# Kernel optimization log

Hardware: AMD Instinct MI355X
Metric: run time of the kernel (lower is better)

The kernel has to match this reference:

```python
import jax, jax.numpy as jnp
import numpy as np

B, S, D, H = 32, 128, 64, 4
HD = D // H            # head dim 16
HT = 4 * D             # hidden_t_dim = 256
TE = 4 * HT            # time_embed_dim = 1024
V = 1024               # vocab
STEP = 0.1             # step_size (Lie-Trotter step)


def setup_inputs():
    key = jax.random.key(0)
    ks = jax.random.split(key, 12)
    n = lambda k, shp: 0.02 * jax.random.normal(k, shp, jnp.float32)
    return dict(
        inputs_idx=jax.random.randint(ks[0], (B, S), 0, V),
        num_loops=100,
        wte=n(ks[1], (V, D)),
        wpe=n(ks[2], (S, D)),
        t_w1=n(ks[3], (HT, TE)), t_b1=jnp.zeros((TE,), jnp.float32),
        t_w2=n(ks[4], (TE, D)), t_b2=jnp.zeros((D,), jnp.float32),
        ln1_g=jnp.ones((D,), jnp.float32), ln1_b=jnp.zeros((D,), jnp.float32),
        w_qkv=n(ks[5], (D, 3 * D)), b_qkv=jnp.zeros((3 * D,), jnp.float32),
        w_o=n(ks[6], (D, D)), b_o=jnp.zeros((D,), jnp.float32),
        ln2_g=jnp.ones((D,), jnp.float32), ln2_b=jnp.zeros((D,), jnp.float32),
        w_fc=n(ks[7], (D, 4 * D)), b_fc=jnp.zeros((4 * D,), jnp.float32),
        w_pr=n(ks[8], (4 * D, D)), b_pr=jnp.zeros((D,), jnp.float32),
        lnf_g=jnp.ones((D,), jnp.float32), lnf_b=jnp.zeros((D,), jnp.float32),
    )


def _ln(x, g, b, eps=1e-5):
    mu = jnp.mean(x, axis=-1, keepdims=True)
    var = jnp.var(x, axis=-1, keepdims=True)
    return (x - mu) * jax.lax.rsqrt(var + eps) * g + b


def _timestep_embedding(t, dim):
    # sinusoidal (diffusion-style) embedding of scalar step index t -> (dim,)
    half = dim // 2
    freqs = jnp.exp(-np.log(10000.0) * jnp.arange(half, dtype=jnp.float32) / half)
    args = t * freqs
    return jnp.concatenate([jnp.cos(args), jnp.sin(args)], axis=-1)


def reference(inputs_idx, num_loops, wte, wpe, t_w1, t_b1, t_w2, t_b2,
              ln1_g, ln1_b, w_qkv, b_qkv, w_o, b_o,
              ln2_g, ln2_b, w_fc, b_fc, w_pr, b_pr, lnf_g, lnf_b):
    x = wte[inputs_idx] + wpe[jnp.arange(S)]          # (B,S,D)
    neg_inf = jnp.float32(-1e9)
    cmask = jnp.where(jnp.tril(jnp.ones((S, S), bool)), 0.0, neg_inf)  # causal
    scale = 1.0 / np.sqrt(HD)

    def step(x, t):
        # shared time embedding added to state each loop iteration
        te = _timestep_embedding(t, HT)
        temb = jax.nn.silu(te @ t_w1 + t_b1) @ t_w2 + t_b2   # (D,)
        x = x + temb
        # pre-norm attention, Lie-Trotter sub-step
        h = _ln(x, ln1_g, ln1_b)
        qkv = h @ w_qkv + b_qkv                               # (B,S,3D)
        q, k, v = jnp.split(qkv, 3, axis=-1)
        q = q.reshape(B, S, H, HD)
        k = k.reshape(B, S, H, HD)
        v = v.reshape(B, S, H, HD)
        att = jnp.einsum('bqhd,bkhd->bhqk', q, k) * scale + cmask
        att = jax.nn.softmax(att, axis=-1)
        a = jnp.einsum('bhqk,bkhd->bqhd', att, v).reshape(B, S, D)
        x = x + STEP * (a @ w_o + b_o)
        # pre-norm MLP, second sub-step
        h = _ln(x, ln2_g, ln2_b)
        m = jax.nn.gelu(h @ w_fc + b_fc) @ w_pr + b_pr
        x = x + STEP * m
        return x, None

    ts = jnp.arange(num_loops, dtype=jnp.float32)
    x, _ = jax.lax.scan(step, x, ts)
    return _ln(x, lnf_g, lnf_b)
```

## Files before the change

kernel.cpp:

```cpp
#include <hip/hip_runtime.h>
#include <hip/hip_bf16.h>
#include <math.h>

#define BB   32
#define SS   128
#define DD   64
#define HTT  256
#define TEE  1024
#define NTHR 512
#define XST  68
#define STEPF 0.1f

typedef __attribute__((ext_vector_type(8))) short short8b;
typedef __attribute__((ext_vector_type(4))) float float4v;

__device__ __forceinline__ unsigned short f2b(float f) {
    union { float f; unsigned int u; } x; x.f = f;
    unsigned int u = x.u + 0x7FFFu + ((x.u >> 16) & 1u);
    return (unsigned short)(u >> 16);
}

__global__ void pack_frags(const float* __restrict__ w_qkv,
                           const float* __restrict__ w_o,
                           const float* __restrict__ w_fc,
                           const float* __restrict__ w_pr,
                           unsigned short* __restrict__ frags) {
    const int tile = blockIdx.x;
    const int t = threadIdx.x;
    const int lane = t >> 3, e = t & 7;
    const float* W; int N, nt, ks;
    if (tile < 24)      { W = w_qkv; N = 192; int s = tile;      nt = s >> 1; ks = s & 1; }
    else if (tile < 32) { W = w_o;   N = 64;  int s = tile - 24; nt = s >> 1; ks = s & 1; }
    else if (tile < 64) { W = w_fc;  N = 256; int s = tile - 32; nt = s >> 1; ks = s & 1; }
    else                { W = w_pr;  N = 64;  int s = tile - 64; nt = s >> 3; ks = s & 7; }
    const int k   = ks * 32 + (lane >> 4) * 8 + e;
    const int col = nt * 16 + (lane & 15);
    frags[tile * 512 + lane * 8 + e] = f2b(W[k * N + col]);
}

__global__ void temb_precompute(const int* __restrict__ nloops_p,
                                const float* __restrict__ t_w1,
                                const float* __restrict__ t_b1,
                                const float* __restrict__ t_w2,
                                const float* __restrict__ t_b2,
                                float* __restrict__ tembBuf) {
    const int t = blockIdx.x;
    const int nl = nloops_p[0];
    if (t >= nl) return;

    __shared__ float te_s[HTT];
    __shared__ float h1[TEE];
    const int tid = threadIdx.x;
    const float tf = (float)t;

    {
        int fi = (tid < 128) ? tid : (tid - 128);
        float freq = expf(-9.210340371976184f * (float)fi * (1.0f / 128.0f));
        float arg = tf * freq;
        te_s[tid] = (tid < 128) ? cosf(arg) : sinf(arg);
    }
    __syncthreads();

    for (int j = tid; j < TEE; j += 256) {
        float acc = t_b1[j];
        for (int i = 0; i < HTT; ++i)
            acc = fmaf(te_s[i], t_w1[i * TEE + j], acc);
        h1[j] = acc / (1.0f + expf(-acc));
    }
    __syncthreads();

    {
        const int d = tid >> 2, part = tid & 3;
        float acc = 0.0f;
        for (int j = part; j < TEE; j += 4)
            acc = fmaf(h1[j], t_w2[j * DD + d], acc);
        acc += __shfl_xor(acc, 1);
        acc += __shfl_xor(acc, 2);
        if (part == 0) tembBuf[t * DD + d] = acc + t_b2[d];
    }
}

__device__ __forceinline__ float gelu_tanh(float u) {
    float z = 0.7978845608028654f * (u + 0.044715f * u * u * u);
    float e = __expf(2.0f * z);
    float th = 1.0f - 2.0f / (e + 1.0f);
    return 0.5f * u * (1.0f + th);
}

__global__ __launch_bounds__(NTHR, 2)
void looped_tf(const int* __restrict__ idx,
               const int* __restrict__ nloops_p,
               const float* __restrict__ wte,
               const float* __restrict__ wpe,
               const float* __restrict__ ln1_g, const float* __restrict__ ln1_b,
               const float* __restrict__ b_qkv,
               const float* __restrict__ b_o,
               const float* __restrict__ ln2_g, const float* __restrict__ ln2_b,
               const float* __restrict__ b_fc,
               const float* __restrict__ b_pr,
               const float* __restrict__ lnf_g, const float* __restrict__ lnf_b,
               const float* __restrict__ tembBuf,
               const unsigned short* __restrict__ frags,
               float* __restrict__ out) {
    __shared__ __align__(16) float xs[SS * XST];
    __shared__ __align__(16) unsigned short hsb[SS * DD];
    __shared__ __align__(16) unsigned char pool[66560];
    __shared__ __align__(16) unsigned short pstage[8 * 640];
    __shared__ __align__(16) unsigned short wfrag[16384];

    unsigned char* qb  = pool;
    unsigned char* kb  = pool + 24576;
    unsigned char* vtb = pool + 49152;
    unsigned short* msb = (unsigned short*)pool;

    const unsigned short* fcF = frags + 32 * 512;
    const unsigned short* prF = frags + 64 * 512;

    const int b   = blockIdx.x;
    const int tid = threadIdx.x;
    const int nl  = nloops_p[0];
    const int wv  = tid >> 6;
    const int ln  = tid & 63;
    const int fr  = ln & 15;
    const int fq  = ln >> 4;

    for (int i = tid; i < 2048; i += NTHR)
        ((int4*)wfrag)[i] = ((const int4*)frags)[i];

    for (int i = tid; i < SS * DD; i += NTHR) {
        int s = i >> 6, d = i & 63;
        xs[s * XST + d] = wte[idx[b * SS + s] * DD + d] + wpe[i];
    }
    __syncthreads();

    const int tok4 = tid >> 2, sub4 = tid & 3;

    auto ln_to_hsb = [&](const float* __restrict__ g, const float* __restrict__ be) {
        float v[16];
        const float* xp = xs + tok4 * XST + sub4 * 16;
        float s1 = 0.f, s2 = 0.f;
#pragma unroll
        for (int r = 0; r < 4; ++r) {
            float4 f = *(const float4*)(xp + 4 * r);
            v[4*r+0]=f.x; v[4*r+1]=f.y; v[4*r+2]=f.z; v[4*r+3]=f.w;
            s1 += f.x + f.y + f.z + f.w;
            s2 += f.x*f.x + f.y*f.y + f.z*f.z + f.w*f.w;
        }
        s1 += __shfl_xor(s1, 1); s2 += __shfl_xor(s2, 1);
        s1 += __shfl_xor(s1, 2); s2 += __shfl_xor(s2, 2);
        float mu = s1 * (1.0f / 64.0f);
        float var = s2 * (1.0f / 64.0f) - mu * mu;
        float rs = rsqrtf(var + 1e-5f);
        short8b p0, p1;
#pragma unroll
        for (int i = 0; i < 8; ++i) {
            int d2 = sub4 * 16 + i;
            p0[i] = (short)f2b((v[i] - mu) * rs * g[d2] + be[d2]);
        }
#pragma unroll
        for (int i = 0; i < 8; ++i) {
            int d2 = sub4 * 16 + 8 + i;
            p1[i] = (short)f2b((v[8+i] - mu) * rs * g[d2] + be[d2]);
        }
        const int row = tok4, swz = (row & 7) << 4;
        char* base = (char*)hsb;
        int b0 = row * 128 + sub4 * 32;
        *(short8b*)(base + (b0 ^ swz)) = p0;
        *(short8b*)(base + ((b0 + 16) ^ swz)) = p1;
    };

    auto load_afrag = [&](const unsigned short* buf, int rstrideB, int kstep) -> short8b {
        int row = wv * 16 + fr;
        int byte = row * rstrideB + kstep * 64 + fq * 16;
        return *(const short8b*)((const char*)buf + (byte ^ ((row & 7) << 4)));
    };

    for (int t = 0; t < nl; ++t) {
        for (int i = tid; i < SS * DD; i += NTHR)
            xs[(i >> 6) * XST + (i & 63)] += tembBuf[t * DD + (i & 63)];
        __syncthreads();

        ln_to_hsb(ln1_g, ln1_b);
        __syncthreads();

        {
            short8b a0 = load_afrag(hsb, 128, 0);
            short8b a1 = load_afrag(hsb, 128, 1);
            float4v acc[12];
#pragma unroll
            for (int nt = 0; nt < 12; ++nt) acc[nt] = (float4v)0.0f;
#pragma unroll
            for (int nt = 0; nt < 12; ++nt) {
                short8b b0 = *(const short8b*)(&wfrag[(nt * 2 + 0) * 512 + ln * 8]);
                short8b b1 = *(const short8b*)(&wfrag[(nt * 2 + 1) * 512 + ln * 8]);
                acc[nt] = __builtin_amdgcn_mfma_f32_16x16x32_bf16(a0, b0, acc[nt], 0, 0, 0);
                acc[nt] = __builtin_amdgcn_mfma_f32_16x16x32_bf16(a1, b1, acc[nt], 0, 0, 0);
            }
#pragma unroll
            for (int nt = 0; nt < 12; ++nt) {
                const int col = nt * 16 + fr;
                const float bias = b_qkv[col];
#pragma unroll
                for (int r = 0; r < 4; ++r) {
                    int row = wv * 16 + fq * 4 + r;
                    unsigned short bv = f2b(acc[nt][r] + bias);
                    if (nt < 4) {
                        int h = nt, d = fr;
                        int byte = h * 6144 + row * 48 + d * 2;
                        byte ^= ((row >> 3) & 7) << 4;
                        *(unsigned short*)(qb + byte) = bv;
                    } else if (nt < 8) {
                        int h = nt - 4, d = fr;
                        *(unsigned short*)(kb + h * 6144 + row * 48 + d * 2) = bv;
                    } else {
                        int h = nt - 8, d = fr;
                        *(unsigned short*)(vtb + h * 4352 + d * 272 + row * 2) = bv;
                    }
                }
            }
        }
        __syncthreads();

        {
            short8b aq[4];
            {
                bool lo = (ln < 32);
#pragma unroll
                for (int h = 0; h < 4; ++h) {
                    short8b z = (short8b)(short)0;
                    if (lo) {
                        int q = wv + 8 * fr;
                        int byte = h * 6144 + q * 48 + (fq & 1) * 16;
                        byte ^= (fr & 7) << 4;
                        z = *(const short8b*)(qb + byte);
                    }
                    aq[h] = z;
                }
            }
            short8b onesb;
#pragma unroll
            for (int e = 0; e < 8; ++e) onesb[e] = (short)0x3F80;

            float4v o[4], lac[4];
#pragma unroll
            for (int h = 0; h < 4; ++h) { o[h] = (float4v)0.0f; lac[h] = (float4v)0.0f; }

            unsigned short* pst = pstage + wv * 640;

            for (int ktp = 0; ktp < 4; ++ktp) {
#pragma unroll
                for (int h = 0; h < 4; ++h) {
                    short8b bk0 = (short8b)(short)0, bk1 = (short8b)(short)0;
                    if (ln < 32) {
                        int kbase = h * 6144 + (fq & 1) * 16;
                        bk0 = *(const short8b*)(kb + kbase + (ktp * 32 + fr) * 48);
                        bk1 = *(const short8b*)(kb + kbase + (ktp * 32 + 16 + fr) * 48);
                    }
                    float4v s0 = __builtin_amdgcn_mfma_f32_16x16x32_bf16(aq[h], bk0, (float4v)0.0f, 0, 0, 0);
                    float4v s1 = __builtin_amdgcn_mfma_f32_16x16x32_bf16(aq[h], bk1, (float4v)0.0f, 0, 0, 0);
#pragma unroll
                    for (int r = 0; r < 4; ++r) {
                        int j = 4 * fq + r;
                        int q = wv + 8 * j;
                        int kk0 = ktp * 32 + fr;
                        int kk1 = kk0 + 16;
                        float p0 = (kk0 <= q) ? __expf(s0[r] * 0.25f) : 0.0f;
                        float p1 = (kk1 <= q) ? __expf(s1[r] * 0.25f) : 0.0f;
                        pst[j * 40 + fr]      = f2b(p0);
                        pst[j * 40 + 16 + fr] = f2b(p1);
                    }
                    short8b ap = *(const short8b*)((const char*)pst + fr * 80 + fq * 16);
                    short8b bv = *(const short8b*)(vtb + h * 4352 + fr * 272 + ktp * 64 + fq * 16);
                    o[h]   = __builtin_amdgcn_mfma_f32_16x16x32_bf16(ap, bv, o[h], 0, 0, 0);
                    lac[h] = __builtin_amdgcn_mfma_f32_16x16x32_bf16(ap, onesb, lac[h], 0, 0, 0);
                }
            }
#pragma unroll
            for (int h = 0; h < 4; ++h) {
#pragma unroll
                for (int r = 0; r < 4; ++r) {
                    int j = 4 * fq + r;
                    int q = wv + 8 * j;
                    float val = o[h][r] / lac[h][r];
                    int byte = (q * 128 + (h * 16 + fr) * 2) ^ ((q & 7) << 4);
                    *(unsigned short*)((char*)hsb + byte) = f2b(val);
                }
            }
        }
        __syncthreads();

        {
            short8b a0 = load_afrag(hsb, 128, 0);
            short8b a1 = load_afrag(hsb, 128, 1);
            float4v acc[4];
#pragma unroll
            for (int nt = 0; nt < 4; ++nt) acc[nt] = (float4v)0.0f;
#pragma unroll
            for (int nt = 0; nt < 4; ++nt) {
                short8b b0 = *(const short8b*)(&wfrag[(24 + nt * 2 + 0) * 512 + ln * 8]);
                short8b b1 = *(const short8b*)(&wfrag[(24 + nt * 2 + 1) * 512 + ln * 8]);
                acc[nt] = __builtin_amdgcn_mfma_f32_16x16x32_bf16(a0, b0, acc[nt], 0, 0, 0);
                acc[nt] = __builtin_amdgcn_mfma_f32_16x16x32_bf16(a1, b1, acc[nt], 0, 0, 0);
            }
#pragma unroll
            for (int nt = 0; nt < 4; ++nt) {
                const int col = nt * 16 + fr;
                const float bias = b_o[col];
#pragma unroll
                for (int r = 0; r < 4; ++r) {
                    int row = wv * 16 + fq * 4 + r;
                    xs[row * XST + col] += STEPF * (acc[nt][r] + bias);
                }
            }
        }
        __syncthreads();

        ln_to_hsb(ln2_g, ln2_b);
        __syncthreads();

        {
            short8b a0 = load_afrag(hsb, 128, 0);
            short8b a1 = load_afrag(hsb, 128, 1);
            float4v acc[16];
#pragma unroll
            for (int nt = 0; nt < 16; ++nt) acc[nt] = (float4v)0.0f;
#pragma unroll
            for (int half = 0; half < 2; ++half) {
                short8b buf[16];
#pragma unroll
                for (int i = 0; i < 16; ++i)
                    buf[i] = *(const short8b*)(fcF + ((half * 16 + i) * 64 + ln) * 8);
#pragma unroll
                for (int i = 0; i < 8; ++i) {
                    int nt = half * 8 + i;
                    acc[nt] = __builtin_amdgcn_mfma_f32_16x16x32_bf16(a0, buf[2*i],   acc[nt], 0, 0, 0);
                    acc[nt] = __builtin_amdgcn_mfma_f32_16x16x32_bf16(a1, buf[2*i+1], acc[nt], 0, 0, 0);
                }
            }
            char* base = (char*)msb;
#pragma unroll
            for (int nt = 0; nt < 16; ++nt) {
                const int col = nt * 16 + fr;
                const float bias = b_fc[col];
#pragma unroll
                for (int r = 0; r < 4; ++r) {
                    int row = wv * 16 + fq * 4 + r;
                    int byte = row * 512 + col * 2;
                    *(unsigned short*)(base + (byte ^ ((row & 7) << 4))) =
                        f2b(gelu_tanh(acc[nt][r] + bias));
                }
            }
        }
        __syncthreads();

        {
            short8b am[8];
#pragma unroll
            for (int ks = 0; ks < 8; ++ks)
                am[ks] = load_afrag(msb, 512, ks);
            float4v acc[4];
#pragma unroll
            for (int nt = 0; nt < 4; ++nt) acc[nt] = (float4v)0.0f;
#pragma unroll
            for (int half = 0; half < 2; ++half) {
                short8b buf[16];
#pragma unroll
                for (int i = 0; i < 16; ++i)
                    buf[i] = *(const short8b*)(prF + ((half * 16 + i) * 64 + ln) * 8);
#pragma unroll
                for (int i = 0; i < 16; ++i) {
                    int nt = half * 2 + (i >> 3);
                    acc[nt] = __builtin_amdgcn_mfma_f32_16x16x32_bf16(am[i & 7], buf[i], acc[nt], 0, 0, 0);
                }
            }
#pragma unroll
            for (int nt = 0; nt < 4; ++nt) {
                const int col = nt * 16 + fr;
                const float bias = b_pr[col];
#pragma unroll
                for (int r = 0; r < 4; ++r) {
                    int row = wv * 16 + fq * 4 + r;
                    xs[row * XST + col] += STEPF * (acc[nt][r] + bias);
                }
            }
        }
        __syncthreads();
    }

    {
        float v[16];
        const float* xp = xs + tok4 * XST + sub4 * 16;
        float s1 = 0.f, s2 = 0.f;
#pragma unroll
        for (int r = 0; r < 4; ++r) {
            float4 f = *(const float4*)(xp + 4 * r);
            v[4*r+0]=f.x; v[4*r+1]=f.y; v[4*r+2]=f.z; v[4*r+3]=f.w;
            s1 += f.x + f.y + f.z + f.w;
            s2 += f.x*f.x + f.y*f.y + f.z*f.z + f.w*f.w;
        }
        s1 += __shfl_xor(s1, 1); s2 += __shfl_xor(s2, 1);
        s1 += __shfl_xor(s1, 2); s2 += __shfl_xor(s2, 2);
        float mu = s1 * (1.0f / 64.0f);
        float var = s2 * (1.0f / 64.0f) - mu * mu;
        float rs = rsqrtf(var + 1e-5f);
        float* op = out + b * SS * DD + tok4 * DD + sub4 * 16;
#pragma unroll
        for (int r = 0; r < 4; ++r) {
            float4 f;
            int d2 = sub4 * 16 + 4 * r;
            f.x = (v[4*r+0] - mu) * rs * lnf_g[d2+0] + lnf_b[d2+0];
            f.y = (v[4*r+1] - mu) * rs * lnf_g[d2+1] + lnf_b[d2+1];
            f.z = (v[4*r+2] - mu) * rs * lnf_g[d2+2] + lnf_b[d2+2];
            f.w = (v[4*r+3] - mu) * rs * lnf_g[d2+3] + lnf_b[d2+3];
            *(float4*)(op + 4 * r) = f;
        }
    }
}

extern "C" void kernel_launch(void* const* d_in, const int* in_sizes, int n_in,
                              void* d_out, int out_size, void* d_ws, size_t ws_size,
                              hipStream_t stream) {
    const int*   idx    = (const int*)  d_in[0];
    const int*   nloops = (const int*)  d_in[1];
    const float* wte    = (const float*)d_in[2];
    const float* wpe    = (const float*)d_in[3];
    const float* t_w1   = (const float*)d_in[4];
    const float* t_b1   = (const float*)d_in[5];
    const float* t_w2   = (const float*)d_in[6];
    const float* t_b2   = (const float*)d_in[7];
    const float* ln1_g  = (const float*)d_in[8];
    const float* ln1_b  = (const float*)d_in[9];
    const float* w_qkv  = (const float*)d_in[10];
    const float* b_qkv  = (const float*)d_in[11];
    const float* w_o    = (const float*)d_in[12];
    const float* b_o    = (const float*)d_in[13];
    const float* ln2_g  = (const float*)d_in[14];
    const float* ln2_b  = (const float*)d_in[15];
    const float* w_fc   = (const float*)d_in[16];
    const float* b_fc   = (const float*)d_in[17];
    const float* w_pr   = (const float*)d_in[18];
    const float* b_pr   = (const float*)d_in[19];
    const float* lnf_g  = (const float*)d_in[20];
    const float* lnf_b  = (const float*)d_in[21];

    float* tembBuf = (float*)d_ws;
    unsigned short* frags = (unsigned short*)((char*)d_ws + 32768);

    pack_frags<<<96, 512, 0, stream>>>(w_qkv, w_o, w_fc, w_pr, frags);
    temb_precompute<<<128, 256, 0, stream>>>(nloops, t_w1, t_b1, t_w2, t_b2, tembBuf);
    looped_tf<<<BB, NTHR, 0, stream>>>(idx, nloops, wte, wpe, ln1_g, ln1_b,
                                       b_qkv, b_o, ln2_g, ln2_b,
                                       b_fc, b_pr, lnf_g, lnf_b,
                                       tembBuf, frags, (float*)d_out);
}
```

Before: 3.838 ms.

## Keep residual stream in MFMA-layout registers and fuse layernorm into GEMM epilogues

The residual state moves from the shared-memory xs array into per-thread registers laid out to match the MFMA output fragments. Layernorm becomes a 16-lane shuffle reduction fused into the attention-output and MLP-projection epilogues, which removes the separate temb-add and LN passes and several block-wide barriers per loop. Biases and LN parameters are hoisted into registers, and K and the P staging buffer are re-laid out so the two softmax probabilities are packed into one 32-bit store. The costs are higher register pressure under the 2-blocks-per-SM launch bound, and correctness now depends on the new K row permutation matching the causal-mask indices.

Result: no change. 3.855 ms (+0.4%).

```diff
diff --git a/kernel.cpp b/kernel.cpp
--- a/kernel.cpp
+++ b/kernel.cpp
@@ -8,7 +8,6 @@
 #define HTT  256
 #define TEE  1024
 #define NTHR 512
-#define XST  68
 #define STEPF 0.1f
 
 typedef __attribute__((ext_vector_type(8))) short short8b;
@@ -18,6 +17,9 @@
     union { float f; unsigned int u; } x; x.f = f;
     unsigned int u = x.u + 0x7FFFu + ((x.u >> 16) & 1u);
     return (unsigned short)(u >> 16);
+}
+__device__ __forceinline__ unsigned int pack2(float lo, float hi) {
+    return (unsigned int)f2b(lo) | ((unsigned int)f2b(hi) << 16);
 }
 
 __global__ void pack_frags(const float* __restrict__ w_qkv,
@@ -102,10 +104,9 @@
                const float* __restrict__ tembBuf,
                const unsigned short* __restrict__ frags,
                float* __restrict__ out) {
-    __shared__ __align__(16) float xs[SS * XST];
     __shared__ __align__(16) unsigned short hsb[SS * DD];
     __shared__ __align__(16) unsigned char pool[66560];
-    __shared__ __align__(16) unsigned short pstage[8 * 640];
+    __shared__ __align__(16) unsigned char pstage[8 * 1152];
     __shared__ __align__(16) unsigned short wfrag[16384];
 
     unsigned char* qb  = pool;
@@ -123,50 +124,66 @@
     const int ln  = tid & 63;
     const int fr  = ln & 15;
     const int fq  = ln >> 4;
+    const int rowbase = wv * 16 + fq * 4;
 
     for (int i = tid; i < 2048; i += NTHR)
         ((int4*)wfrag)[i] = ((const int4*)frags)[i];
 
-    for (int i = tid; i < SS * DD; i += NTHR) {
-        int s = i >> 6, d = i & 63;
-        xs[s * XST + d] = wte[idx[b * SS + s] * DD + d] + wpe[i];
-    }
+    float bqkvr[12], bor[4], bprr[4];
+    float l1g[4], l1b[4], l2g[4], l2b[4], lfg[4], lfb[4];
+#pragma unroll
+    for (int nt = 0; nt < 12; ++nt) bqkvr[nt] = b_qkv[nt * 16 + fr];
+#pragma unroll
+    for (int nc = 0; nc < 4; ++nc) {
+        int c = nc * 16 + fr;
+        bor[nc] = b_o[c];  bprr[nc] = b_pr[c];
+        l1g[nc] = ln1_g[c]; l1b[nc] = ln1_b[c];
+        l2g[nc] = ln2_g[c]; l2b[nc] = ln2_b[c];
+        lfg[nc] = lnf_g[c]; lfb[nc] = lnf_b[c];
+    }
+
+    float xr[4][4];
+#pragma unroll
+    for (int r = 0; r < 4; ++r) {
+        int row = rowbase + r;
+        int iv = idx[b * SS + row];
+#pragma unroll
+        for (int nc = 0; nc < 4; ++nc)
+            xr[r][nc] = wte[iv * 64 + nc * 16 + fr] + wpe[row * 64 + nc * 16 + fr];
+    }
+
     __syncthreads();
 
-    const int tok4 = tid >> 2, sub4 = tid & 3;
-
-    auto ln_to_hsb = [&](const float* __restrict__ g, const float* __restrict__ be) {
-        float v[16];
-        const float* xp = xs + tok4 * XST + sub4 * 16;
-        float s1 = 0.f, s2 = 0.f;
+    auto ln_fused = [&](const float* g4, const float* b4) {
+        float s1[4], s2[4];
 #pragma unroll
         for (int r = 0; r < 4; ++r) {
-            float4 f = *(const float4*)(xp + 4 * r);
-            v[4*r+0]=f.x; v[4*r+1]=f.y; v[4*r+2]=f.z; v[4*r+3]=f.w;
-            s1 += f.x + f.y + f.z + f.w;
-            s2 += f.x*f.x + f.y*f.y + f.z*f.z + f.w*f.w;
-        }
-        s1 += __shfl_xor(s1, 1); s2 += __shfl_xor(s2, 1);
-        s1 += __shfl_xor(s1, 2); s2 += __shfl_xor(s2, 2);
-        float mu = s1 * (1.0f / 64.0f);
-        float var = s2 * (1.0f / 64.0f) - mu * mu;
-        float rs = rsqrtf(var + 1e-5f);
-        short8b p0, p1;
-#pragma unroll
-        for (int i = 0; i < 8; ++i) {
-            int d2 = sub4 * 16 + i;
-            p0[i] = (short)f2b((v[i] - mu) * rs * g[d2] + be[d2]);
-        }
-#pragma unroll
-        for (int i = 0; i < 8; ++i) {
-            int d2 = sub4 * 16 + 8 + i;
-            p1[i] = (short)f2b((v[8+i] - mu) * rs * g[d2] + be[d2]);
-        }
-        const int row = tok4, swz = (row & 7) << 4;
-        char* base = (char*)hsb;
-        int b0 = row * 128 + sub4 * 32;
-        *(short8b*)(base + (b0 ^ swz)) = p0;
-        *(short8b*)(base + ((b0 + 16) ^ swz)) = p1;
+            s1[r] = xr[r][0] + xr[r][1] + xr[r][2] + xr[r][3];
+            s2[r] = xr[r][0]*xr[r][0] + xr[r][1]*xr[r][1]
+                  + xr[r][2]*xr[r][2] + xr[r][3]*xr[r][3];
+        }
+#pragma unroll
+        for (int m = 1; m <= 8; m <<= 1) {
+#pragma unroll
+            for (int r = 0; r < 4; ++r) {
+                s1[r] += __shfl_xor(s1[r], m);
+                s2[r] += __shfl_xor(s2[r], m);
+            }
+        }
+#pragma unroll
+        for (int r = 0; r < 4; ++r) {
+            float mu = s1[r] * (1.0f / 64.0f);
+            float var = s2[r] * (1.0f / 64.0f) - mu * mu;
+            float rs = rsqrtf(var + 1e-5f);
+            int row = rowbase + r;
+            int swz = (row & 7) << 4;
+#pragma unroll
+            for (int nc = 0; nc < 4; ++nc) {
+                float h = (xr[r][nc] - mu) * rs * g4[nc] + b4[nc];
+                int byte = (row * 128 + (nc * 16 + fr) * 2) ^ swz;
+                *(unsigned short*)((char*)hsb + byte) = f2b(h);
+            }
+        }
     };
 
     auto load_afrag = [&](const unsigned short* buf, int rstrideB, int kstep) -> short8b {
@@ -175,14 +192,17 @@
         return *(const short8b*)((const char*)buf + (byte ^ ((row & 7) << 4)));
     };
 
+    if (nl > 0) {
+#pragma unroll
+        for (int nc = 0; nc < 4; ++nc) {
+            float tv = tembBuf[nc * 16 + fr];
+#pragma unroll
+            for (int r = 0; r < 4; ++r) xr[r][nc] += tv;
+        }
+        ln_fused(l1g, l1b);
+    }
+
     for (int t = 0; t < nl; ++t) {
-        for (int i = tid; i < SS * DD; i += NTHR)
-            xs[(i >> 6) * XST + (i & 63)] += tembBuf[t * DD + (i & 63)];
-        __syncthreads();
-
-        ln_to_hsb(ln1_g, ln1_b);
-        __syncthreads();
-
         {
             short8b a0 = load_afrag(hsb, 128, 0);
             short8b a1 = load_afrag(hsb, 128, 1);
@@ -198,23 +218,21 @@
             }
 #pragma unroll
             for (int nt = 0; nt < 12; ++nt) {
-                const int col = nt * 16 + fr;
-                const float bias = b_qkv[col];
 #pragma unroll
                 for (int r = 0; r < 4; ++r) {
-                    int row = wv * 16 + fq * 4 + r;
-                    unsigned short bv = f2b(acc[nt][r] + bias);
+                    int row = rowbase + r;
+                    unsigned short bv = f2b(acc[nt][r] + bqkvr[nt]);
                     if (nt < 4) {
-                        int h = nt, d = fr;
-                        int byte = h * 6144 + row * 48 + d * 2;
+                        int byte = nt * 6144 + row * 48 + fr * 2;
                         byte ^= ((row >> 3) & 7) << 4;
                         *(unsigned short*)(qb + byte) = bv;
                     } else if (nt < 8) {
-                        int h = nt - 4, d = fr;
-                        *(unsigned short*)(kb + h * 6144 + row * 48 + d * 2) = bv;
+                        int h = nt - 4;
+                        int p = (row >> 1) + 64 * (row & 1);
+                        *(unsigned short*)(kb + h * 6144 + p * 48 + fr * 2) = bv;
                     } else {
-                        int h = nt - 8, d = fr;
-                        *(unsigned short*)(vtb + h * 4352 + d * 272 + row * 2) = bv;
+                        int h = nt - 8;
+                        *(unsigned short*)(vtb + h * 4352 + fr * 272 + row * 2) = bv;
                     }
                 }
             }
@@ -245,7 +263,7 @@
 #pragma unroll
             for (int h = 0; h < 4; ++h) { o[h] = (float4v)0.0f; lac[h] = (float4v)0.0f; }
 
-            unsigned short* pst = pstage + wv * 640;
+            unsigned char* pst = pstage + wv * 1152;
 
             for (int ktp = 0; ktp < 4; ++ktp) {
 #pragma unroll
@@ -253,8 +271,8 @@
                     short8b bk0 = (short8b)(short)0, bk1 = (short8b)(short)0;
                     if (ln < 32) {
                         int kbase = h * 6144 + (fq & 1) * 16;
-                        bk0 = *(const short8b*)(kb + kbase + (ktp * 32 + fr) * 48);
-                        bk1 = *(const short8b*)(kb + kbase + (ktp * 32 + 16 + fr) * 48);
+                        bk0 = *(const short8b*)(kb + kbase + (ktp * 16 + fr) * 48);
+                        bk1 = *(const short8b*)(kb + kbase + (64 + ktp * 16 + fr) * 48);
                     }
                     float4v s0 = __builtin_amdgcn_mfma_f32_16x16x32_bf16(aq[h], bk0, (float4v)0.0f, 0, 0, 0);
                     float4v s1 = __builtin_amdgcn_mfma_f32_16x16x32_bf16(aq[h], bk1, (float4v)0.0f, 0, 0, 0);
@@ -262,14 +280,12 @@
                     for (int r = 0; r < 4; ++r) {
                         int j = 4 * fq + r;
                         int q = wv + 8 * j;
-                        int kk0 = ktp * 32 + fr;
-                        int kk1 = kk0 + 16;
-                        float p0 = (kk0 <= q) ? __expf(s0[r] * 0.25f) : 0.0f;
-                        float p1 = (kk1 <= q) ? __expf(s1[r] * 0.25f) : 0.0f;
-                        pst[j * 40 + fr]      = f2b(p0);
-                        pst[j * 40 + 16 + fr] = f2b(p1);
+                        int k0 = ktp * 32 + 2 * fr;
+                        float p0 = (k0     <= q) ? __expf(s0[r] * 0.25f) : 0.0f;
+                        float p1 = (k0 + 1 <= q) ? __expf(s1[r] * 0.25f) : 0.0f;
+                        *(unsigned int*)(pst + j * 72 + fr * 4) = pack2(p0, p1);
                     }
-                    short8b ap = *(const short8b*)((const char*)pst + fr * 80 + fq * 16);
+                    short8b ap = *(const short8b*)(pst + fr * 72 + fq * 16);
                     short8b bv = *(const short8b*)(vtb + h * 4352 + fr * 272 + ktp * 64 + fq * 16);
                     o[h]   = __builtin_amdgcn_mfma_f32_16x16x32_bf16(ap, bv, o[h], 0, 0, 0);
                     lac[h] = __builtin_amdgcn_mfma_f32_16x16x32_bf16(ap, onesb, lac[h], 0, 0, 0);
@@ -303,20 +319,12 @@
                 acc[nt] = __builtin_amdgcn_mfma_f32_16x16x32_bf16(a1, b1, acc[nt], 0, 0, 0);
             }
 #pragma unroll
-            for (int nt = 0; nt < 4; ++nt) {
-                const int col = nt * 16 + fr;
-                const float bias = b_o[col];
-#pragma unroll
-                for (int r = 0; r < 4; ++r) {
-                    int row = wv * 16 + fq * 4 + r;
-                    xs[row * XST + col] += STEPF * (acc[nt][r] + bias);
-                }
-            }
-        }
-        __syncthreads();
-
-        ln_to_hsb(ln2_g, ln2_b);
-        __syncthreads();
+            for (int nt = 0; nt < 4; ++nt)
+#pragma unroll
+                for (int r = 0; r < 4; ++r)
+                    xr[r][nt] += STEPF * (acc[nt][r] + bor[nt]);
+            ln_fused(l2g, l2b);
+        }
 
         {
             short8b a0 = load_afrag(hsb, 128, 0);
@@ -340,79 +348,89 @@
             char* base = (char*)msb;
 #pragma unroll
             for (int nt = 0; nt < 16; ++nt) {
-                const int col = nt * 16 + fr;
-                const float bias = b_fc[col];
+                const float bias = b_fc[nt * 16 + fr];
 #pragma unroll
                 for (int r = 0; r < 4; ++r) {
-                    int row = wv * 16 + fq * 4 + r;
-                    int byte = row * 512 + col * 2;
+                    int row = rowbase + r;
+                    int byte = row * 512 + (nt * 16 + fr) * 2;
                     *(unsigned short*)(base + (byte ^ ((row & 7) << 4))) =
                         f2b(gelu_tanh(acc[nt][r] + bias));
                 }
             }
         }
-        __syncthreads();
 
         {
             short8b am[8];
 #pragma unroll
             for (int ks = 0; ks < 8; ++ks)
                 am[ks] = load_afrag(msb, 512, ks);
+            short8b buf0[16], buf1[16];
+#pragma unroll
+            for (int i = 0; i < 16; ++i)
+                buf0[i] = *(const short8b*)(prF + (i * 64 + ln) * 8);
+#pragma unroll
+            for (int i = 0; i < 16; ++i)
+                buf1[i] = *(const short8b*)(prF + ((16 + i) * 64 + ln) * 8);
+            __syncthreads();
+
             float4v acc[4];
 #pragma unroll
             for (int nt = 0; nt < 4; ++nt) acc[nt] = (float4v)0.0f;
 #pragma unroll
-            for (int half = 0; half < 2; ++half) {
-                short8b buf[16];
-#pragma unroll
-                for (int i = 0; i < 16; ++i)
-                    buf[i] = *(const short8b*)(prF + ((half * 16 + i) * 64 + ln) * 8);
-#pragma unroll
-                for (int i = 0; i < 16; ++i) {
-                    int nt = half * 2 + (i >> 3);
-                    acc[nt] = __builtin_amdgcn_mfma_f32_16x16x32_bf16(am[i & 7], buf[i], acc[nt], 0, 0, 0);
-                }
-            }
-#pragma unroll
-            for (int nt = 0; nt < 4; ++nt) {
-                const int col = nt * 16 + fr;
-                const float bias = b_pr[col];
-#pragma unroll
-                for (int r = 0; r < 4; ++r) {
-                    int row = wv * 16 + fq * 4 + r;
-                    xs[row * XST + col] += STEPF * (acc[nt][r] + bias);
-                }
-            }
-        }
-        __syncthreads();
+            for (int i = 0; i < 16; ++i) {
+                int nt = i >> 3;
+                acc[nt] = __builtin_amdgcn_mfma_f32_16x16x32_bf16(am[i & 7], buf0[i], acc[nt], 0, 0, 0);
+            }
+#pragma unroll
+            for (int i = 0; i < 16; ++i) {
+                int nt = 2 + (i >> 3);
+                acc[nt] = __builtin_amdgcn_mfma_f32_16x16x32_bf16(am[i & 7], buf1[i], acc[nt], 0, 0, 0);
+            }
+#pragma unroll
+            for (int nt = 0; nt < 4; ++nt)
+#pragma unroll
+                for (int r = 0; r < 4; ++r)
+                    xr[r][nt] += STEPF * (acc[nt][r] + bprr[nt]);
+
+            if (t + 1 < nl) {
+#pragma unroll
+                for (int nc = 0; nc < 4; ++nc) {
+                    float tv = tembBuf[(t + 1) * 64 + nc * 16 + fr];
+#pragma unroll
+                    for (int r = 0; r < 4; ++r) xr[r][nc] += tv;
+                }
+                ln_fused(l1g, l1b);
+            }
+        }
     }
 
     {
-        float v[16];
-        const float* xp = xs + tok4 * XST + sub4 * 16;
-        float s1 = 0.f, s2 = 0.f;
+        float s1[4], s2[4];
 #pragma unroll
         for (int r = 0; r < 4; ++r) {
-            float4 f = *(const float4*)(xp + 4 * r);
-            v[4*r+0]=f.x; v[4*r+1]=f.y; v[4*r+2]=f.z; v[4*r+3]=f.w;
-            s1 += f.x + f.y + f.z + f.w;
-            s2 += f.x*f.x + f.y*f.y + f.z*f.z + f.w*f.w;
-        }
-        s1 += __shfl_xor(s1, 1); s2 += __shfl_xor(s2, 1);
-        s1 += __shfl_xor(s1, 2); s2 += __shfl_xor(s2, 2);
-        float mu = s1 * (1.0f / 64.0f);
-        float var = s2 * (1.0f / 64.0f) - mu * mu;
-        float rs = rsqrtf(var + 1e-5f);
-        float* op = out + b * SS * DD + tok4 * DD + sub4 * 16;
+            s1[r] = xr[r][0] + xr[r][1] + xr[r][2] + xr[r][3];
+            s2[r] = xr[r][0]*xr[r][0] + xr[r][1]*xr[r][1]
+                  + xr[r][2]*xr[r][2] + xr[r][3]*xr[r][3];
+        }
+#pragma unroll
+        for (int m = 1; m <= 8; m <<= 1) {
+#pragma unroll
+            for (int r = 0; r < 4; ++r) {
+                s1[r] += __shfl_xor(s1[r], m);
+                s2[r] += __shfl_xor(s2[r], m);
+            }
+        }
 #pragma unroll
         for (int r = 0; r < 4; ++r) {
-            float4 f;
-            int d2 = sub4 * 16 + 4 * r;
-            f.x = (v[4*r+0] - mu) * rs * lnf_g[d2+0] + lnf_b[d2+0];
-            f.y = (v[4*r+1] - mu) * rs * lnf_g[d2+1] + lnf_b[d2+1];
-            f.z = (v[4*r+2] - mu) * rs * lnf_g[d2+2] + lnf_b[d2+2];
-            f.w = (v[4*r+3] - mu) * rs * lnf_g[d2+3] + lnf_b[d2+3];
-            *(float4*)(op + 4 * r) = f;
+            float mu = s1[r] * (1.0f / 64.0f);
+            float var = s2[r] * (1.0f / 64.0f) - mu * mu;
+            float rs = rsqrtf(var + 1e-5f);
+            int row = rowbase + r;
+#pragma unroll
+            for (int nc = 0; nc < 4; ++nc) {
+                float val = (xr[r][nc] - mu) * rs * lfg[nc] + lfb[nc];
+                out[b * SS * DD + row * 64 + nc * 16 + fr] = val;
+            }
         }
     }
 }
```
